# Performance work log

Hardware: AMD Instinct MI355X
Metric: run time of the kernel (lower is better)

The kernel has to match this reference:

```python
import jax, jax.numpy as jnp
import numpy as np

B, T, LA, L = 4, 32, 32, 512
D, H, C = 2048, 16, 128
KV_DIM = 2048
K = T * LA  # total kv tokens per batch element
EPS = 1e-5


def _ln(x):
    m = jnp.mean(x, axis=-1, keepdims=True)
    v = jnp.var(x, axis=-1, keepdims=True)
    return (x - m) * jax.lax.rsqrt(v + EPS)


def setup_inputs() -> dict:
    key = jax.random.key(0)
    ks = jax.random.split(key, 10)
    s = 1.0 / np.sqrt(D)
    sk = 1.0 / np.sqrt(KV_DIM)
    return {
        "x": jax.random.normal(ks[0], (B, T, LA, KV_DIM), jnp.float32),
        "latents": jax.random.normal(ks[1], (B, L, D), jnp.float32),
        "t_emb": jax.random.normal(ks[2], (B, 3, D), jnp.float32) * 0.02,
        "q_lens": jnp.full((B,), L, dtype=jnp.int32),
        "k_lens": jax.random.randint(ks[3], (B,), K // 2, K + 1).astype(jnp.int32),
        "ln_kv_w": jnp.ones((KV_DIM,), jnp.float32),
        "ln_kv_b": jnp.zeros((KV_DIM,), jnp.float32),
        "ssg": jax.random.normal(ks[4], (1, 3, D), jnp.float32) * s,  # shift_scale_gate param (adaLN=True)
        "Wq": jax.random.normal(ks[5], (D, D), jnp.float32) * s,
        "bq": jnp.zeros((D,), jnp.float32),
        "Wkv": jax.random.normal(ks[6], (KV_DIM, 2 * D), jnp.float32) * sk,
        "bkv": jnp.zeros((2 * D,), jnp.float32),
        "Wo": jax.random.normal(ks[7], (D, D), jnp.float32) * s,
        "bo": jnp.zeros((D,), jnp.float32),
    }


def reference(x, latents, t_emb, q_lens, k_lens, ln_kv_w, ln_kv_b, ssg,
              Wq, bq, Wkv, bkv, Wo, bo):
    # norm_kv (affine LayerNorm over kv_dim)
    xk = _ln(x) * ln_kv_w + ln_kv_b  # (B,T,LA,KV_DIM)
    # AdaLN modulate: shift/scale/gate from t_emb + learned shift_scale_gate
    mod = t_emb + ssg  # (B,3,D)
    shift, scale, gate = mod[:, 0:1], mod[:, 1:2], mod[:, 2:3]  # (B,1,D)
    norm_q = _ln(latents)  # norm_q has no affine when adaLN=True
    lat = norm_q * (1.0 + scale) + shift
    # projections
    q = (lat @ Wq + bq).reshape(B, L, H, C)
    kv = (xk.reshape(B, K, KV_DIM) @ Wkv + bkv)  # (B,K,2D)
    k, v = kv[..., :D], kv[..., D:]
    k = k.reshape(B, K, H, C)
    v = v.reshape(B, K, H, C)
    # varlen attention == per-batch masked attention (keys beyond k_lens masked)
    scores = jnp.einsum("blhc,bkhc->bhlk", q, k) / np.sqrt(C)
    kmask = jnp.arange(K)[None, :] < k_lens[:, None]  # (B,K)
    scores = jnp.where(kmask[:, None, None, :], scores, jnp.finfo(scores.dtype).min)
    attn = jax.nn.softmax(scores, axis=-1)
    out = jnp.einsum("bhlk,bkhc->blhc", attn, v).reshape(B, L, D)
    # queries beyond q_lens are invalid -> zero them (varlen packing semantics)
    qmask = (jnp.arange(L)[None, :] < q_lens[:, None])[..., None]  # (B,L,1)
    out = out * qmask
    return (out @ Wo + bo) * gate
```

## Files before the change

### kernel.cpp

```cpp
#include <hip/hip_runtime.h>

typedef unsigned short u16;
typedef short bf16x8 __attribute__((ext_vector_type(8)));
typedef float f32x4 __attribute__((ext_vector_type(4)));

#define MFMA_BF16(a, b, c) __builtin_amdgcn_mfma_f32_16x16x32_bf16((a), (b), (c), 0, 0, 0)
#define ATT_SCALE 0.08838834764831845f

__device__ __forceinline__ u16 f2bf(float f) {
  union { float f; unsigned int u; } cv;
  cv.f = f;
  unsigned int u = cv.u + 0x7fffu + ((cv.u >> 16) & 1u);
  return (u16)(u >> 16);
}

__global__ __launch_bounds__(256) void prep_kernel(
    const float* __restrict__ x, const float* __restrict__ ln_w,
    const float* __restrict__ ln_b, const float* __restrict__ latents,
    const float* __restrict__ t_emb, const float* __restrict__ ssg,
    const float* __restrict__ Wq, const float* __restrict__ Wo,
    const float* __restrict__ Wkv,
    u16* __restrict__ xk_out, u16* __restrict__ lat_out,
    u16* __restrict__ WqT, u16* __restrict__ WoT, u16* __restrict__ WkvT)
{
  __shared__ float shmem[32 * 33];
  const int blk = blockIdx.x;
  const int tid = threadIdx.x;
  if (blk < 6144) {
    const bool is_x = blk < 4096;
    const int row = is_x ? blk : blk - 4096;
    const float* src = is_x ? (x + (size_t)row * 2048) : (latents + (size_t)row * 2048);
    const float4* xr = (const float4*)src;
    float4 v0 = xr[tid];
    float4 v1 = xr[tid + 256];
    float sum = v0.x + v0.y + v0.z + v0.w + v1.x + v1.y + v1.z + v1.w;
    float sq  = v0.x*v0.x + v0.y*v0.y + v0.z*v0.z + v0.w*v0.w
              + v1.x*v1.x + v1.y*v1.y + v1.z*v1.z + v1.w*v1.w;
    #pragma unroll
    for (int off = 32; off > 0; off >>= 1) {
      sum += __shfl_xor(sum, off);
      sq  += __shfl_xor(sq, off);
    }
    if ((tid & 63) == 0) { shmem[tid >> 6] = sum; shmem[(tid >> 6) + 4] = sq; }
    __syncthreads();
    sum = shmem[0] + shmem[1] + shmem[2] + shmem[3];
    sq  = shmem[4] + shmem[5] + shmem[6] + shmem[7];
    const float mean = sum * (1.0f / 2048.0f);
    const float var  = sq * (1.0f / 2048.0f) - mean * mean;
    const float rstd = rsqrtf(var + 1e-5f);
    if (is_x) {
      const float4* w4 = (const float4*)ln_w;
      const float4* b4 = (const float4*)ln_b;
      ushort4* orow = (ushort4*)(xk_out + (size_t)row * 2048);
      #pragma unroll
      for (int j = 0; j < 2; ++j) {
        const int idx = tid + j * 256;
        const float4 v = j ? v1 : v0;
        const float4 ww = w4[idx];
        const float4 bb = b4[idx];
        ushort4 o;
        o.x = f2bf((v.x - mean) * rstd * ww.x + bb.x);
        o.y = f2bf((v.y - mean) * rstd * ww.y + bb.y);
        o.z = f2bf((v.z - mean) * rstd * ww.z + bb.z);
        o.w = f2bf((v.w - mean) * rstd * ww.w + bb.w);
        orow[idx] = o;
      }
    } else {
      const int bidx = row >> 9;
      const float4* te = (const float4*)(t_emb + (size_t)bidx * 3 * 2048);
      const float4* sg = (const float4*)ssg;
      ushort4* orow = (ushort4*)(lat_out + (size_t)row * 2048);
      #pragma unroll
      for (int j = 0; j < 2; ++j) {
        const int idx = tid + j * 256;
        const float4 v = j ? v1 : v0;
        const float4 t0 = te[idx];
        const float4 t1 = te[512 + idx];
        const float4 s0 = sg[idx];
        const float4 s1 = sg[512 + idx];
        ushort4 o;
        o.x = f2bf(((v.x - mean) * rstd) * (1.0f + t1.x + s1.x) + (t0.x + s0.x));
        o.y = f2bf(((v.y - mean) * rstd) * (1.0f + t1.y + s1.y) + (t0.y + s0.y));
        o.z = f2bf(((v.z - mean) * rstd) * (1.0f + t1.z + s1.z) + (t0.z + s0.z));
        o.w = f2bf(((v.w - mean) * rstd) * (1.0f + t1.w + s1.w) + (t0.w + s0.w));
        orow[idx] = o;
      }
    }
  } else {
    int t = blk - 6144;
    const float* in;
    u16* outp;
    int C, cx, ry;
    if (t < 4096)      { in = Wq;  outp = WqT;  C = 2048; cx = t & 63;  ry = t >> 6; }
    else if (t < 8192) { t -= 4096; in = Wo;  outp = WoT;  C = 2048; cx = t & 63;  ry = t >> 6; }
    else               { t -= 8192; in = Wkv; outp = WkvT; C = 4096; cx = t & 127; ry = t >> 7; }
    float (*tile)[33] = (float(*)[33])shmem;
    const int R = 2048;
    const int c0 = cx * 32;
    const int r0 = ry * 32;
    const int tx = tid & 31;
    const int ty = tid >> 5;
    #pragma unroll
    for (int i = 0; i < 4; ++i)
      tile[ty + i * 8][tx] = in[(size_t)(r0 + ty + i * 8) * C + c0 + tx];
    __syncthreads();
    #pragma unroll
    for (int i = 0; i < 4; ++i)
      outp[(size_t)(c0 + ty + i * 8) * R + r0 + tx] = f2bf(tile[tx][ty + i * 8]);
  }
}

template<int BM>
__global__ __launch_bounds__(256) void gemm_bf16_kernel(
    const u16* __restrict__ A, const u16* __restrict__ BT,
    int Kd, int mode,
    const float* __restrict__ bias,
    u16* __restrict__ out_q, u16* __restrict__ out_k, u16* __restrict__ out_vT,
    float* __restrict__ out_f,
    const float* __restrict__ t_emb, const float* __restrict__ ssg,
    const int* __restrict__ k_lens)
{
  constexpr int TI = BM / 32;
  __shared__ u16 As[2][BM][40];
  __shared__ u16 Bs[2][128][40];
  const int tid  = threadIdx.x;
  const int lane = tid & 63;
  const int wv   = tid >> 6;
  const int wm   = wv & 1, wn = wv >> 1;
  const int quad = lane >> 4, lq = lane & 15;
  const int m0 = blockIdx.y * BM, n0 = blockIdx.x * 128;

  f32x4 acc[TI][4];
  #pragma unroll
  for (int i = 0; i < TI; ++i)
    #pragma unroll
    for (int j = 0; j < 4; ++j)
      acc[i][j] = (f32x4){0.f, 0.f, 0.f, 0.f};

  int kiters = Kd;
  if (mode == 1 && (m0 & 1023) >= k_lens[m0 >> 10]) kiters = 0;

  const int rB  = tid >> 1;
  const int hfB = (tid & 1) * 16;
  const u16* gB = BT + (size_t)(n0 + rB) * Kd + hfB;
  const int rA  = (BM == 128) ? (tid >> 1) : (tid >> 2);
  const int hA  = (BM == 128) ? 0 : ((tid >> 1) & 1);
  const int hfA = (tid & 1) * 16;
  const u16* gA = A + (size_t)(m0 + rA) * Kd + hA * 32 + hfA;

  for (int k0 = 0; k0 < kiters; k0 += 64) {
    uint4 a00, a01, a10, a11;
    a00 = *(const uint4*)(gA + k0);
    a01 = *(const uint4*)(gA + k0 + 8);
    if (BM == 128) {
      a10 = *(const uint4*)(gA + k0 + 32);
      a11 = *(const uint4*)(gA + k0 + 40);
    }
    const uint4 b00 = *(const uint4*)(gB + k0);
    const uint4 b01 = *(const uint4*)(gB + k0 + 8);
    const uint4 b10 = *(const uint4*)(gB + k0 + 32);
    const uint4 b11 = *(const uint4*)(gB + k0 + 40);
    __syncthreads();
    *(uint4*)&As[hA][rA][hfA]     = a00;
    *(uint4*)&As[hA][rA][hfA + 8] = a01;
    if (BM == 128) {
      *(uint4*)&As[1][rA][hfA]     = a10;
      *(uint4*)&As[1][rA][hfA + 8] = a11;
    }
    *(uint4*)&Bs[0][rB][hfB]     = b00;
    *(uint4*)&Bs[0][rB][hfB + 8] = b01;
    *(uint4*)&Bs[1][rB][hfB]     = b10;
    *(uint4*)&Bs[1][rB][hfB + 8] = b11;
    __syncthreads();
    #pragma unroll
    for (int kk = 0; kk < 2; ++kk) {
      bf16x8 av[TI], bv[4];
      #pragma unroll
      for (int i = 0; i < TI; ++i)
        av[i] = *(const bf16x8*)&As[kk][wm * (BM / 2) + i * 16 + lq][quad * 8];
      #pragma unroll
      for (int j = 0; j < 4; ++j)
        bv[j] = *(const bf16x8*)&Bs[kk][wn * 64 + j * 16 + lq][quad * 8];
      #pragma unroll
      for (int i = 0; i < TI; ++i)
        #pragma unroll
        for (int j = 0; j < 4; ++j)
          acc[i][j] = MFMA_BF16(av[i], bv[j], acc[i][j]);
    }
  }

  #pragma unroll
  for (int i = 0; i < TI; ++i) {
    const int mlb = m0 + wm * (BM / 2) + i * 16 + quad * 4;
    #pragma unroll
    for (int j = 0; j < 4; ++j) {
      const int n = n0 + wn * 64 + j * 16 + lq;
      const float bs = bias[n];
      if (mode == 0) {
        const int h = n >> 7, c = n & 127;
        #pragma unroll
        for (int rr = 0; rr < 4; ++rr) {
          const int m = mlb + rr;
          const int bb = m >> 9, l = m & 511;
          out_q[((size_t)(bb * 16 + h) * 512 + l) * 128 + c] =
              f2bf((acc[i][j][rr] + bs) * ATT_SCALE);
        }
      } else if (mode == 1) {
        if (n < 2048) {
          const int h = n >> 7, c = n & 127;
          #pragma unroll
          for (int rr = 0; rr < 4; ++rr) {
            const int m = mlb + rr;
            const int bb = m >> 10, kk = m & 1023;
            out_k[((size_t)(bb * 16 + h) * 1024 + kk) * 128 + c] = f2bf(acc[i][j][rr] + bs);
          }
        } else {
          const int n2 = n - 2048;
          const int h = n2 >> 7, c = n2 & 127;
          const int bb = mlb >> 10, kk = mlb & 1023;
          ushort4 o4;
          o4.x = f2bf(acc[i][j][0] + bs);
          o4.y = f2bf(acc[i][j][1] + bs);
          o4.z = f2bf(acc[i][j][2] + bs);
          o4.w = f2bf(acc[i][j][3] + bs);
          *(ushort4*)&out_vT[((size_t)(bb * 16 + h) * 128 + c) * 1024 + kk] = o4;
        }
      } else {
        #pragma unroll
        for (int rr = 0; rr < 4; ++rr) {
          const int m = mlb + rr;
          const int bb = m >> 9;
          const float g = t_emb[((size_t)bb * 3 + 2) * 2048 + n] + ssg[2 * 2048 + n];
          out_f[(size_t)m * 2048 + n] = (acc[i][j][rr] + bs) * g;
        }
      }
    }
  }
}

__global__ __launch_bounds__(256) void attn_kernel(
    const u16* __restrict__ qb, const u16* __restrict__ kb,
    const u16* __restrict__ vT, const int* __restrict__ k_lens,
    const int* __restrict__ q_lens, u16* __restrict__ ao)
{
  __shared__ u16 Ks[64][132];
  __shared__ u16 Vs[128][68];
  __shared__ u16 Ps[64][68];
  const int tid  = threadIdx.x;
  const int w    = tid >> 6;
  const int lane = tid & 63;
  const int quad = lane >> 4, lq = lane & 15;
  const int bh = blockIdx.y;
  const int b  = bh >> 4;
  const int l0 = blockIdx.x * 64;
  const int kl = k_lens[b];
  const int ql = q_lens[b];

  bf16x8 qf[4];
  {
    const u16* qp = qb + ((size_t)bh * 512 + l0 + w * 16 + lq) * 128 + quad * 8;
    #pragma unroll
    for (int ks = 0; ks < 4; ++ks)
      qf[ks] = *(const bf16x8*)(qp + ks * 32);
  }

  const int krow = tid >> 4;
  const int kcol = tid & 15;
  const u16* kg = kb + ((size_t)bh * 1024 + krow) * 128 + kcol * 8;
  const int vrow = tid >> 3;
  const int vcol = tid & 7;
  const u16* vg = vT + (size_t)bh * 128 * 1024 + (size_t)vrow * 1024 + vcol * 8;

  f32x4 o[8];
  #pragma unroll
  for (int j = 0; j < 8; ++j) o[j] = (f32x4){0.f, 0.f, 0.f, 0.f};
  float mrun[4], lrun[4];
  #pragma unroll
  for (int rr = 0; rr < 4; ++rr) { mrun[rr] = -__builtin_inff(); lrun[rr] = 0.f; }

  const int nkt = (kl + 63) >> 6;
  uint4 kd[4], vd[4];
  #pragma unroll
  for (int p = 0; p < 4; ++p)
    kd[p] = *(const uint4*)(kg + (size_t)(p * 16) * 128);
  #pragma unroll
  for (int p = 0; p < 4; ++p)
    vd[p] = *(const uint4*)(vg + (size_t)p * 32 * 1024);

  for (int kt = 0; kt < nkt; ++kt) {
    __syncthreads();
    #pragma unroll
    for (int p = 0; p < 4; ++p)
      *(uint4*)&Ks[krow + p * 16][kcol * 8] = kd[p];
    #pragma unroll
    for (int p = 0; p < 4; ++p)
      *(uint4*)&Vs[vrow + p * 32][vcol * 8] = vd[p];
    __syncthreads();

    if (kt + 1 < nkt) {
      const int kn = (kt + 1) * 64;
      #pragma unroll
      for (int p = 0; p < 4; ++p)
        kd[p] = *(const uint4*)(kg + (size_t)(kn + p * 16) * 128);
      #pragma unroll
      for (int p = 0; p < 4; ++p)
        vd[p] = *(const uint4*)(vg + (size_t)p * 32 * 1024 + kn);
    }

    const int k0 = kt * 64;
    f32x4 s[4];
    #pragma unroll
    for (int ct = 0; ct < 4; ++ct) {
      s[ct] = (f32x4){0.f, 0.f, 0.f, 0.f};
      #pragma unroll
      for (int ks = 0; ks < 4; ++ks) {
        const bf16x8 kf = *(const bf16x8*)&Ks[ct * 16 + lq][ks * 32 + quad * 8];
        s[ct] = MFMA_BF16(qf[ks], kf, s[ct]);
      }
    }
    #pragma unroll
    for (int ct = 0; ct < 4; ++ct) {
      const bool valid = (k0 + ct * 16 + lq) < kl;
      #pragma unroll
      for (int rr = 0; rr < 4; ++rr)
        s[ct][rr] = valid ? s[ct][rr] : -__builtin_inff();
    }
    float mnew[4], alpha[4], rs[4];
    #pragma unroll
    for (int rr = 0; rr < 4; ++rr) {
      float tm = fmaxf(fmaxf(s[0][rr], s[1][rr]), fmaxf(s[2][rr], s[3][rr]));
      tm = fmaxf(tm, __shfl_xor(tm, 1));
      tm = fmaxf(tm, __shfl_xor(tm, 2));
      tm = fmaxf(tm, __shfl_xor(tm, 4));
      tm = fmaxf(tm, __shfl_xor(tm, 8));
      const float mn = fmaxf(mrun[rr], tm);
      alpha[rr] = __expf(mrun[rr] - mn);
      mrun[rr] = mn;
      mnew[rr] = mn;
      rs[rr] = 0.f;
    }
    #pragma unroll
    for (int ct = 0; ct < 4; ++ct)
      #pragma unroll
      for (int rr = 0; rr < 4; ++rr) {
        const float p = __expf(s[ct][rr] - mnew[rr]);
        s[ct][rr] = p;
        rs[rr] += p;
      }
    #pragma unroll
    for (int rr = 0; rr < 4; ++rr) {
      float t = rs[rr];
      t += __shfl_xor(t, 1);
      t += __shfl_xor(t, 2);
      t += __shfl_xor(t, 4);
      t += __shfl_xor(t, 8);
      lrun[rr] = lrun[rr] * alpha[rr] + t;
    }
    #pragma unroll
    for (int j = 0; j < 8; ++j)
      #pragma unroll
      for (int rr = 0; rr < 4; ++rr)
        o[j][rr] *= alpha[rr];

    #pragma unroll
    for (int ct = 0; ct < 4; ++ct)
      #pragma unroll
      for (int rr = 0; rr < 4; ++rr)
        Ps[w * 16 + quad * 4 + rr][ct * 16 + lq] = f2bf(s[ct][rr]);

    bf16x8 pf[2];
    pf[0] = *(const bf16x8*)&Ps[w * 16 + lq][quad * 8];
    pf[1] = *(const bf16x8*)&Ps[w * 16 + lq][32 + quad * 8];

    #pragma unroll
    for (int j = 0; j < 8; ++j) {
      #pragma unroll
      for (int kk = 0; kk < 2; ++kk) {
        const bf16x8 vf = *(const bf16x8*)&Vs[j * 16 + lq][kk * 32 + quad * 8];
        o[j] = MFMA_BF16(pf[kk], vf, o[j]);
      }
    }
  }

  const int h = bh & 15;
  #pragma unroll
  for (int rr = 0; rr < 4; ++rr) {
    const int row = l0 + w * 16 + quad * 4 + rr;
    const float inv = (row < ql) ? (1.0f / lrun[rr]) : 0.0f;
    u16* op = ao + ((size_t)b * 512 + row) * 2048 + h * 128 + lq;
    #pragma unroll
    for (int j = 0; j < 8; ++j)
      op[j * 16] = f2bf(o[j][rr] * inv);
  }
}

extern "C" void kernel_launch(void* const* d_in, const int* in_sizes, int n_in,
                              void* d_out, int out_size, void* d_ws, size_t ws_size,
                              hipStream_t stream) {
  (void)in_sizes; (void)n_in; (void)out_size; (void)ws_size;
  const float* x       = (const float*)d_in[0];
  const float* latents = (const float*)d_in[1];
  const float* t_emb   = (const float*)d_in[2];
  const int*   q_lens  = (const int*)d_in[3];
  const int*   k_lens  = (const int*)d_in[4];
  const float* ln_w    = (const float*)d_in[5];
  const float* ln_b    = (const float*)d_in[6];
  const float* ssg     = (const float*)d_in[7];
  const float* Wq      = (const float*)d_in[8];
  const float* bq      = (const float*)d_in[9];
  const float* Wkv     = (const float*)d_in[10];
  const float* bkv     = (const float*)d_in[11];
  const float* Wo      = (const float*)d_in[12];
  const float* bo      = (const float*)d_in[13];
  float* out = (float*)d_out;

  u16* ws = (u16*)d_ws;
  const size_t MEG = (size_t)1 << 20;
  u16* WqT  = ws;
  u16* WoT  = ws + 4  * MEG;
  u16* WkvT = ws + 8  * MEG;
  u16* xk   = ws + 16 * MEG;
  u16* lat  = ws + 24 * MEG;
  u16* qb   = ws + 28 * MEG;
  u16* kbuf = ws + 32 * MEG;
  u16* vTb  = ws + 40 * MEG;
  u16* aob  = ws + 48 * MEG;

  prep_kernel<<<dim3(22528), dim3(256), 0, stream>>>(
      x, ln_w, ln_b, latents, t_emb, ssg, Wq, Wo, Wkv,
      xk, lat, WqT, WoT, WkvT);

  gemm_bf16_kernel<64><<<dim3(16, 32), dim3(256), 0, stream>>>(
      lat, WqT, 2048, 0, bq, qb, nullptr, nullptr, nullptr, nullptr, nullptr, k_lens);
  gemm_bf16_kernel<128><<<dim3(32, 32), dim3(256), 0, stream>>>(
      xk, WkvT, 2048, 1, bkv, nullptr, kbuf, vTb, nullptr, nullptr, nullptr, k_lens);

  attn_kernel<<<dim3(8, 64), dim3(256), 0, stream>>>(qb, kbuf, vTb, k_lens, q_lens, aob);

  gemm_bf16_kernel<64><<<dim3(16, 32), dim3(256), 0, stream>>>(
      aob, WoT, 2048, 2, bo, nullptr, nullptr, nullptr, out, t_emb, ssg, k_lens);
}
```

Measured before the change: 422.3 us.

## Replace KV projection GEMM with 256x256-tile pipelined kernel using direct global-to-LDS loads

The KV projection moves from the generic 128x128 bf16 GEMM to a dedicated kernel. It uses 256x256 tiles, 512 threads and 128KB of dynamic LDS, and loads tiles with global_load_lds so data goes straight from global memory into swizzled shared memory without passing through registers. The K loop is split into four MFMA phases interleaved with staged loads for the next buffers, coordinated by raw s_barrier, vmcnt waits and s_setprio. The aim is to overlap memory traffic with matrix math and raise data reuse. In exchange, the hand-tuned synchronisation is fragile, and the large LDS footprint limits how many blocks fit per CU.

```diff
diff --git a/kernel.cpp b/kernel.cpp
--- a/kernel.cpp
+++ b/kernel.cpp
@@ -12,6 +12,12 @@
   cv.f = f;
   unsigned int u = cv.u + 0x7fffu + ((cv.u >> 16) & 1u);
   return (u16)(u >> 16);
+}
+
+__device__ __forceinline__ void gload_lds16(const u16* g, u16* l) {
+  __builtin_amdgcn_global_load_lds(
+      (const __attribute__((address_space(1))) unsigned int*)g,
+      (__attribute__((address_space(3))) unsigned int*)l, 16, 0, 0);
 }
 
 __global__ __launch_bounds__(256) void prep_kernel(
@@ -115,10 +121,8 @@
     const u16* __restrict__ A, const u16* __restrict__ BT,
     int Kd, int mode,
     const float* __restrict__ bias,
-    u16* __restrict__ out_q, u16* __restrict__ out_k, u16* __restrict__ out_vT,
-    float* __restrict__ out_f,
-    const float* __restrict__ t_emb, const float* __restrict__ ssg,
-    const int* __restrict__ k_lens)
+    u16* __restrict__ out_q, float* __restrict__ out_f,
+    const float* __restrict__ t_emb, const float* __restrict__ ssg)
 {
   constexpr int TI = BM / 32;
   __shared__ u16 As[2][BM][40];
@@ -137,9 +141,6 @@
     for (int j = 0; j < 4; ++j)
       acc[i][j] = (f32x4){0.f, 0.f, 0.f, 0.f};
 
-  int kiters = Kd;
-  if (mode == 1 && (m0 & 1023) >= k_lens[m0 >> 10]) kiters = 0;
-
   const int rB  = tid >> 1;
   const int hfB = (tid & 1) * 16;
   const u16* gB = BT + (size_t)(n0 + rB) * Kd + hfB;
@@ -148,14 +149,10 @@
   const int hfA = (tid & 1) * 16;
   const u16* gA = A + (size_t)(m0 + rA) * Kd + hA * 32 + hfA;
 
-  for (int k0 = 0; k0 < kiters; k0 += 64) {
-    uint4 a00, a01, a10, a11;
+  for (int k0 = 0; k0 < Kd; k0 += 64) {
+    uint4 a00, a01;
     a00 = *(const uint4*)(gA + k0);
     a01 = *(const uint4*)(gA + k0 + 8);
-    if (BM == 128) {
-      a10 = *(const uint4*)(gA + k0 + 32);
-      a11 = *(const uint4*)(gA + k0 + 40);
-    }
     const uint4 b00 = *(const uint4*)(gB + k0);
     const uint4 b01 = *(const uint4*)(gB + k0 + 8);
     const uint4 b10 = *(const uint4*)(gB + k0 + 32);
@@ -163,10 +160,6 @@
     __syncthreads();
     *(uint4*)&As[hA][rA][hfA]     = a00;
     *(uint4*)&As[hA][rA][hfA + 8] = a01;
-    if (BM == 128) {
-      *(uint4*)&As[1][rA][hfA]     = a10;
-      *(uint4*)&As[1][rA][hfA + 8] = a11;
-    }
     *(uint4*)&Bs[0][rB][hfB]     = b00;
     *(uint4*)&Bs[0][rB][hfB + 8] = b01;
     *(uint4*)&Bs[1][rB][hfB]     = b10;
@@ -205,26 +198,6 @@
           out_q[((size_t)(bb * 16 + h) * 512 + l) * 128 + c] =
               f2bf((acc[i][j][rr] + bs) * ATT_SCALE);
         }
-      } else if (mode == 1) {
-        if (n < 2048) {
-          const int h = n >> 7, c = n & 127;
-          #pragma unroll
-          for (int rr = 0; rr < 4; ++rr) {
-            const int m = mlb + rr;
-            const int bb = m >> 10, kk = m & 1023;
-            out_k[((size_t)(bb * 16 + h) * 1024 + kk) * 128 + c] = f2bf(acc[i][j][rr] + bs);
-          }
-        } else {
-          const int n2 = n - 2048;
-          const int h = n2 >> 7, c = n2 & 127;
-          const int bb = mlb >> 10, kk = mlb & 1023;
-          ushort4 o4;
-          o4.x = f2bf(acc[i][j][0] + bs);
-          o4.y = f2bf(acc[i][j][1] + bs);
-          o4.z = f2bf(acc[i][j][2] + bs);
-          o4.w = f2bf(acc[i][j][3] + bs);
-          *(ushort4*)&out_vT[((size_t)(bb * 16 + h) * 128 + c) * 1024 + kk] = o4;
-        }
       } else {
         #pragma unroll
         for (int rr = 0; rr < 4; ++rr) {
@@ -233,6 +206,163 @@
           const float g = t_emb[((size_t)bb * 3 + 2) * 2048 + n] + ssg[2 * 2048 + n];
           out_f[(size_t)m * 2048 + n] = (acc[i][j][rr] + bs) * g;
         }
+      }
+    }
+  }
+}
+
+#define KV_BARRIER() asm volatile("s_barrier" ::: "memory")
+
+#define KV_MMA(MH, NH, BV)                                                     \
+  do {                                                                         \
+    _Pragma("unroll")                                                          \
+    for (int i = 0; i < 4; ++i) {                                              \
+      _Pragma("unroll")                                                        \
+      for (int j = 0; j < 2; ++j) {                                            \
+        acc[(MH)*4 + i][(NH)*2 + j] =                                          \
+            MFMA_BF16(av[i][0], BV[j][0], acc[(MH)*4 + i][(NH)*2 + j]);        \
+        acc[(MH)*4 + i][(NH)*2 + j] =                                          \
+            MFMA_BF16(av[i][1], BV[j][1], acc[(MH)*4 + i][(NH)*2 + j]);        \
+      }                                                                        \
+    }                                                                          \
+  } while (0)
+
+__global__ __launch_bounds__(512, 2) void gemm_kv_8phase(
+    const u16* __restrict__ A, const u16* __restrict__ BT,
+    const float* __restrict__ bias,
+    u16* __restrict__ out_k, u16* __restrict__ out_vT,
+    const int* __restrict__ k_lens)
+{
+  extern __shared__ __align__(16) u16 lds[];
+  u16* const Alds = lds;
+  u16* const Blds = lds + 32768;
+
+  const int tid  = threadIdx.x;
+  const int lane = tid & 63;
+  const int wv   = tid >> 6;
+  const int wm   = wv >> 2;
+  const int wn   = wv & 3;
+  const int quad = lane >> 4, lq = lane & 15;
+  const int m0 = blockIdx.y * 256, n0 = blockIdx.x * 256;
+
+  f32x4 acc[8][4];
+  #pragma unroll
+  for (int a = 0; a < 8; ++a)
+    #pragma unroll
+    for (int b = 0; b < 4; ++b)
+      acc[a][b] = (f32x4){0.f, 0.f, 0.f, 0.f};
+
+  const int kl = k_lens[m0 >> 10];
+  const bool active = (m0 & 1023) < kl;
+
+  if (active) {
+    const int l3 = lane >> 3;
+    const int sgcol = (((lane & 7) - l3) & 7) * 8;
+    auto stageA = [&](int buf, int mh, int k0) {
+      #pragma unroll
+      for (int p = 0; p < 2; ++p) {
+        const u16* src = A + (size_t)(m0 + p * 128 + mh * 64 + wv * 8 + l3) * 2048 + k0 + sgcol;
+        gload_lds16(src, &Alds[(buf * 2 + mh) * 8192 + (p * 8 + wv) * 512]);
+      }
+    };
+    auto stageB = [&](int buf, int nh, int k0) {
+      #pragma unroll
+      for (int p = 0; p < 2; ++p) {
+        const int c = p * 8 + wv;
+        const u16* src = BT + (size_t)(n0 + (c >> 2) * 64 + nh * 32 + (c & 3) * 8 + l3) * 2048 + k0 + sgcol;
+        gload_lds16(src, &Blds[(buf * 2 + nh) * 8192 + c * 512]);
+      }
+    };
+
+    bf16x8 av[4][2], bv0[2][2], bv1[2][2];
+    const int posk0 = (quad + (lq & 7)) & 7;
+    const int posk1 = (4 + quad + (lq & 7)) & 7;
+    auto read_av = [&](int buf, int mh) {
+      #pragma unroll
+      for (int i = 0; i < 4; ++i) {
+        const int base = (buf * 2 + mh) * 8192 + (wm * 64 + i * 16 + lq) * 64;
+        av[i][0] = *(const bf16x8*)&Alds[base + posk0 * 8];
+        av[i][1] = *(const bf16x8*)&Alds[base + posk1 * 8];
+      }
+    };
+    auto read_bv = [&](int buf, int nh, bf16x8 (*bv)[2]) {
+      #pragma unroll
+      for (int j = 0; j < 2; ++j) {
+        const int base = (buf * 2 + nh) * 8192 + (wn * 32 + j * 16 + lq) * 64;
+        bv[j][0] = *(const bf16x8*)&Blds[base + posk0 * 8];
+        bv[j][1] = *(const bf16x8*)&Blds[base + posk1 * 8];
+      }
+    };
+
+    const int nt = 32;
+    stageA(0, 0, 0); stageB(0, 0, 0); stageA(0, 1, 0); stageB(0, 1, 0);
+    stageA(1, 0, 64); stageB(1, 0, 64); stageA(1, 1, 64);
+    asm volatile("s_waitcnt vmcnt(6)" ::: "memory");
+    KV_BARRIER();
+
+    for (int t = 0; t < nt; ++t) {
+      const int cur = t & 1, nxt = cur ^ 1;
+      read_av(cur, 0);
+      read_bv(cur, 0, bv0);
+      if (t + 1 < nt) stageB(nxt, 1, (t + 1) * 64);
+      KV_BARRIER();
+      __builtin_amdgcn_s_setprio(1);
+      KV_MMA(0, 0, bv0);
+      __builtin_amdgcn_s_setprio(0);
+      KV_BARRIER();
+      read_bv(cur, 1, bv1);
+      if (t + 2 < nt) stageA(cur, 0, (t + 2) * 64);
+      KV_BARRIER();
+      __builtin_amdgcn_s_setprio(1);
+      KV_MMA(0, 1, bv1);
+      __builtin_amdgcn_s_setprio(0);
+      KV_BARRIER();
+      read_av(cur, 1);
+      if (t + 2 < nt) stageB(cur, 0, (t + 2) * 64);
+      KV_BARRIER();
+      __builtin_amdgcn_s_setprio(1);
+      KV_MMA(1, 0, bv0);
+      __builtin_amdgcn_s_setprio(0);
+      KV_BARRIER();
+      if (t + 2 < nt) stageA(cur, 1, (t + 2) * 64);
+      KV_BARRIER();
+      __builtin_amdgcn_s_setprio(1);
+      KV_MMA(1, 1, bv1);
+      __builtin_amdgcn_s_setprio(0);
+      if (t < nt - 2) {
+        asm volatile("s_waitcnt vmcnt(6)" ::: "memory");
+      } else if (t == nt - 2) {
+        asm volatile("s_waitcnt vmcnt(0)" ::: "memory");
+      }
+      KV_BARRIER();
+    }
+  }
+
+  #pragma unroll
+  for (int a = 0; a < 8; ++a) {
+    const int mlb = m0 + wm * 128 + (a >> 2) * 64 + (a & 3) * 16 + quad * 4;
+    #pragma unroll
+    for (int b = 0; b < 4; ++b) {
+      const int n = n0 + wn * 64 + (b >> 1) * 32 + (b & 1) * 16 + lq;
+      const float bs = bias[n];
+      if (n < 2048) {
+        const int h = n >> 7, c = n & 127;
+        #pragma unroll
+        for (int rr = 0; rr < 4; ++rr) {
+          const int m = mlb + rr;
+          const int bb = m >> 10, kk = m & 1023;
+          out_k[((size_t)(bb * 16 + h) * 1024 + kk) * 128 + c] = f2bf(acc[a][b][rr] + bs);
+        }
+      } else {
+        const int n2 = n - 2048;
+        const int h = n2 >> 7, c = n2 & 127;
+        const int bb = mlb >> 10, kk = mlb & 1023;
+        ushort4 o4;
+        o4.x = f2bf(acc[a][b][0] + bs);
+        o4.y = f2bf(acc[a][b][1] + bs);
+        o4.z = f2bf(acc[a][b][2] + bs);
+        o4.w = f2bf(acc[a][b][3] + bs);
+        *(ushort4*)&out_vT[((size_t)(bb * 16 + h) * 128 + c) * 1024 + kk] = o4;
       }
     }
   }
@@ -426,17 +556,20 @@
   u16* vTb  = ws + 40 * MEG;
   u16* aob  = ws + 48 * MEG;
 
+  hipFuncSetAttribute(reinterpret_cast<const void*>(&gemm_kv_8phase),
+                      hipFuncAttributeMaxDynamicSharedMemorySize, 131072);
+
   prep_kernel<<<dim3(22528), dim3(256), 0, stream>>>(
       x, ln_w, ln_b, latents, t_emb, ssg, Wq, Wo, Wkv,
       xk, lat, WqT, WoT, WkvT);
 
   gemm_bf16_kernel<64><<<dim3(16, 32), dim3(256), 0, stream>>>(
-      lat, WqT, 2048, 0, bq, qb, nullptr, nullptr, nullptr, nullptr, nullptr, k_lens);
-  gemm_bf16_kernel<128><<<dim3(32, 32), dim3(256), 0, stream>>>(
-      xk, WkvT, 2048, 1, bkv, nullptr, kbuf, vTb, nullptr, nullptr, nullptr, k_lens);
+      lat, WqT, 2048, 0, bq, qb, nullptr, nullptr, nullptr);
+  gemm_kv_8phase<<<dim3(16, 16), dim3(512), 131072, stream>>>(
+      xk, WkvT, bkv, kbuf, vTb, k_lens);
 
   attn_kernel<<<dim3(8, 64), dim3(256), 0, stream>>>(qb, kbuf, vTb, k_lens, q_lens, aob);
 
   gemm_bf16_kernel<64><<<dim3(16, 32), dim3(256), 0, stream>>>(
-      aob, WoT, 2048, 2, bo, nullptr, nullptr, nullptr, out, t_emb, ssg, k_lens);
-}
+      aob, WoT, 2048, 2, bo, nullptr, out, t_emb, ssg);
+}
```

Measured after the change: 392.3 us. 7.1% less time.
